# Performance work log

Hardware: AMD Instinct MI355X
Metric: run time of the kernel (lower is better)

## Reference

```python
import jax, jax.numpy as jnp
import numpy as np

N = 131072   # total utterances (nodes)
B = 2048     # conversations (segments)
F = 200      # n_features (hard-coded 200 in source)
STEPS = 3    # processing_steps (reason_steps[0])


def setup_inputs() -> dict:
    key = jax.random.key(0)
    k = jax.random.split(key, 8)
    x = jax.random.normal(k[0], (N, F), dtype=jnp.float32)
    batch = jnp.sort(jax.random.randint(k[1], (N,), 0, B, dtype=jnp.int32))
    cos_coef = jax.random.normal(k[2], (N,), dtype=jnp.float32)
    q_star = jax.random.normal(k[3], (B, 2 * F), dtype=jnp.float32)
    s = 1.0 / np.sqrt(F)
    # PyTorch LSTM params: gate order i, f, g, o; input size 2F, hidden F
    W_ih = jax.random.uniform(k[4], (4 * F, 2 * F), jnp.float32, -s, s)
    W_hh = jax.random.uniform(k[5], (4 * F, F), jnp.float32, -s, s)
    b_ih = jax.random.uniform(k[6], (4 * F,), jnp.float32, -s, s)
    b_hh = jax.random.uniform(k[7], (4 * F,), jnp.float32, -s, s)
    return {"x": x, "batch": batch, "cos_coef": cos_coef, "q_star": q_star,
            "W_ih": W_ih, "W_hh": W_hh, "b_ih": b_ih, "b_hh": b_hh}


def _lstm_cell(inp, h, c, W_ih, W_hh, b_ih, b_hh):
    gates = inp @ W_ih.T + b_ih + h @ W_hh.T + b_hh  # [B, 4F]
    i, f, g, o = jnp.split(gates, 4, axis=-1)
    c = jax.nn.sigmoid(f) * c + jax.nn.sigmoid(i) * jnp.tanh(g)
    h = jax.nn.sigmoid(o) * jnp.tanh(c)
    return h, c


def reference(x, batch, cos_coef, q_star, W_ih, W_hh, b_ih, b_hh):
    # initial LSTM hidden: a_sit[i] = cos_row_i @ x[segment_i]  -> segment_sum
    h = jax.ops.segment_sum(cos_coef[:, None] * x, batch, num_segments=B)  # [B,F]
    c = jnp.zeros((B, F), dtype=x.dtype)
    for _ in range(STEPS):
        h, c = _lstm_cell(q_star, h, c, W_ih, W_hh, b_ih, b_hh)
        q = h                                            # [B,F]
        e = jnp.sum(x * q[batch], axis=-1)               # [N]
        m = jax.ops.segment_max(e, batch, num_segments=B)
        ex = jnp.exp(e - m[batch])
        denom = jax.ops.segment_sum(ex, batch, num_segments=B)
        a = ex / denom[batch]                            # per-segment softmax
        r = jax.ops.segment_sum(a[:, None] * x, batch, num_segments=B)  # [B,F]
        q_star = jnp.concatenate([q, r], axis=-1)        # [B,2F]
    return q_star
```

## Files before the change

### kernel.cpp

```cpp
#include <hip/hip_runtime.h>
#include <hip/hip_bf16.h>

#define N_NODES 131072
#define B_SEG   2048
#define F_DIM   200
#define K_DIM   608
#define NEG_INF (-3.4e38f)
#define NMAX    512

typedef __attribute__((ext_vector_type(8))) short bf16x8;
typedef __attribute__((ext_vector_type(4))) float f32x4;

__device__ __forceinline__ float b2f(unsigned short u) {
  union { unsigned int i; float f; } v; v.i = ((unsigned int)u) << 16; return v.f;
}
__device__ __forceinline__ unsigned short f2bu(float f) {
  __hip_bfloat16 h = __float2bfloat16(f);
  return *reinterpret_cast<unsigned short*>(&h);
}
__device__ __forceinline__ float sigmoidf_(float x) { return 1.f / (1.f + __expf(-x)); }
__device__ __forceinline__ float tanhf_(float x) {
  float e = __expf(2.f * x);
  return 1.f - 2.f / (1.f + e);
}
__device__ __forceinline__ int lower_bound_batch(const int* __restrict__ batch, int target) {
  int lo = 0, hi = N_NODES;
  while (lo < hi) {
    int mid = (lo + hi) >> 1;
    if (batch[mid] < target) lo = mid + 1; else hi = mid;
  }
  return lo;
}

__global__ __launch_bounds__(256) void init_kernel(
    const float* __restrict__ xf, const int* __restrict__ batch,
    const float* __restrict__ cosc, const float* __restrict__ qs0,
    const float* __restrict__ Wih, const float* __restrict__ Whh,
    const float* __restrict__ bih, const float* __restrict__ bhh,
    unsigned short* __restrict__ A, unsigned short* __restrict__ Wc,
    float* __restrict__ bsum, int* __restrict__ seg_off) {
  __shared__ float rpart[5][F_DIM];
  __shared__ float cw[NMAX];
  __shared__ int sb[2];
  int b = blockIdx.x, tid = threadIdx.x;
  if (tid < 2) sb[tid] = lower_bound_batch(batch, b + tid);
  int idx = b * 256 + tid;
  if (idx < 832 * K_DIM) {
    int row = idx / K_DIM, k = idx - row * K_DIM;
    float v = 0.f;
    if (row < 800) {
      if (k < 400)      v = Wih[row * 400 + k];
      else if (k < 600) v = Whh[row * 200 + (k - 400)];
    }
    Wc[idx] = f2bu(v);
  }
  if (idx < 800) bsum[idx] = bih[idx] + bhh[idx];
  __syncthreads();
  int start = sb[0], end = sb[1];
  int n = end - start; if (n > NMAX) n = NMAX;
  if (tid == 0) {
    seg_off[b] = start;
    if (b == 0) seg_off[B_SEG] = N_NODES;
  }
  for (int r = tid; r < n; r += 256) cw[r] = cosc[start + r];
  __syncthreads();
  unsigned short* Arow = A + (size_t)b * K_DIM;
  int rgrp = tid / 50, col4 = tid - rgrp * 50;
  float a0 = 0.f, a1 = 0.f, a2 = 0.f, a3 = 0.f;
  if (rgrp < 5) {
    const float* xp = xf + (size_t)start * F_DIM + 4 * col4;
    int r = rgrp;
    float4 v = {0.f, 0.f, 0.f, 0.f};
    if (r < n) v = *(const float4*)(xp + (size_t)r * F_DIM);
    for (; r < n; r += 5) {
      float4 vc = v;
      int rn = r + 5;
      if (rn < n) v = *(const float4*)(xp + (size_t)rn * F_DIM);
      float cv = cw[r];
      a0 += cv * vc.x; a1 += cv * vc.y; a2 += cv * vc.z; a3 += cv * vc.w;
    }
    rpart[rgrp][4 * col4]     = a0;
    rpart[rgrp][4 * col4 + 1] = a1;
    rpart[rgrp][4 * col4 + 2] = a2;
    rpart[rgrp][4 * col4 + 3] = a3;
  }
  if (tid < 100) {
    float4 v = *(const float4*)(qs0 + (size_t)b * 400 + 4 * tid);
    ushort4 o; o.x = f2bu(v.x); o.y = f2bu(v.y); o.z = f2bu(v.z); o.w = f2bu(v.w);
    *(ushort4*)(Arow + 4 * tid) = o;
  }
  if (tid < 8) Arow[600 + tid] = 0;
  __syncthreads();
  if (tid < F_DIM) {
    float acc = rpart[0][tid] + rpart[1][tid] + rpart[2][tid] + rpart[3][tid]
              + rpart[4][tid];
    Arow[400 + tid] = f2bu(acc);
  }
}

__global__ __launch_bounds__(256) void gemm_gates(
    const unsigned short* __restrict__ A, const unsigned short* __restrict__ W,
    float* __restrict__ gates) {
  int tid = threadIdx.x;
  int bm = blockIdx.x * 32, bn = blockIdx.y * 64;
  int wave = tid >> 6, lane = tid & 63;
  int quad = lane >> 4, col = lane & 15;
  int strip = wave >> 1;
  int tp = (wave & 1) * 2;
  f32x4 acc[2];
  acc[0] = (f32x4){0.f, 0.f, 0.f, 0.f};
  acc[1] = (f32x4){0.f, 0.f, 0.f, 0.f};
  const unsigned short* Ap = A + (size_t)(bm + strip * 16 + col) * K_DIM + quad * 8;
  const unsigned short* Wp = W + (size_t)(bn + col) * K_DIM + quad * 8;
#pragma unroll
  for (int k0 = 0; k0 < K_DIM; k0 += 32) {
    bf16x8 af = *(const bf16x8*)(Ap + k0);
#pragma unroll
    for (int t = 0; t < 2; t++) {
      bf16x8 bfr = *(const bf16x8*)(Wp + (size_t)(tp + t) * 16 * K_DIM + k0);
      acc[t] = __builtin_amdgcn_mfma_f32_16x16x32_bf16(af, bfr, acc[t], 0, 0, 0);
    }
  }
#pragma unroll
  for (int t = 0; t < 2; t++) {
    int gn = bn + (tp + t) * 16 + col;
    if (gn < 800) {
#pragma unroll
      for (int r = 0; r < 4; r++) {
        int gm = bm + strip * 16 + quad * 4 + r;
        gates[(size_t)gm * 800 + gn] = acc[t][r];
      }
    }
  }
}

__global__ __launch_bounds__(256) void attn_fused(
    const float* __restrict__ xf, const int* __restrict__ seg_off,
    const float* __restrict__ gates, const float* __restrict__ bsum,
    float* __restrict__ cvec, unsigned short* __restrict__ A,
    float* __restrict__ out, int step) {
  __shared__ float q_s[F_DIM];
  __shared__ float rpart[8][F_DIM];
  __shared__ float redm[8], redl[8];
  int b = blockIdx.x, tid = threadIdx.x;
  int start = seg_off[b], end = seg_off[b + 1];
  int n = end - start;
  unsigned short* Arow = A + (size_t)b * K_DIM;
  if (tid < F_DIM) {
    int f = tid;
    const float* g = gates + (size_t)b * 800;
    float gi = g[f]       + bsum[f];
    float gf = g[200 + f] + bsum[200 + f];
    float gg = g[400 + f] + bsum[400 + f];
    float go = g[600 + f] + bsum[600 + f];
    float cp = (step > 0) ? cvec[(size_t)b * F_DIM + f] : 0.f;
    float cn = sigmoidf_(gf) * cp + sigmoidf_(gi) * tanhf_(gg);
    float hn = sigmoidf_(go) * tanhf_(cn);
    cvec[(size_t)b * F_DIM + f] = cn;
    q_s[f] = hn;
    if (step < 2) {
      unsigned short hb = f2bu(hn);
      Arow[f] = hb;
      Arow[400 + f] = hb;
    }
  }
  __syncthreads();
  int wave = tid >> 6, lane = tid & 63;
  int half = lane >> 5, hl = lane & 31;
  int hw = wave * 2 + half;
  bool act = (hl < 25);
  float q0=0,q1=0,q2=0,q3=0,q4=0,q5=0,q6=0,q7=0;
  if (act) {
    q0 = q_s[8*hl];   q1 = q_s[8*hl+1]; q2 = q_s[8*hl+2]; q3 = q_s[8*hl+3];
    q4 = q_s[8*hl+4]; q5 = q_s[8*hl+5]; q6 = q_s[8*hl+6]; q7 = q_s[8*hl+7];
  }
  const float* xp = xf + (size_t)start * F_DIM + 8 * hl;
  float m = NEG_INF, l = 0.f;
  float a0=0,a1=0,a2=0,a3=0,a4=0,a5=0,a6=0,a7=0;
  int r = hw;
  float4 va = {0.f,0.f,0.f,0.f}, vb = {0.f,0.f,0.f,0.f};
  if (act && r < n) {
    va = *(const float4*)(xp + (size_t)r * F_DIM);
    vb = *(const float4*)(xp + (size_t)r * F_DIM + 4);
  }
  for (; r < n; r += 8) {
    float4 ca = va, cb = vb;
    int rn = r + 8;
    if (act && rn < n) {
      va = *(const float4*)(xp + (size_t)rn * F_DIM);
      vb = *(const float4*)(xp + (size_t)rn * F_DIM + 4);
    }
    float p = act ? (q0*ca.x + q1*ca.y + q2*ca.z + q3*ca.w
                   + q4*cb.x + q5*cb.y + q6*cb.z + q7*cb.w) : 0.f;
#pragma unroll
    for (int off = 16; off; off >>= 1) p += __shfl_xor(p, off, 32);
    float e = p;
    float mn = fmaxf(m, e);
    float fac = __expf(m - mn);
    float w  = __expf(e - mn);
    l  = l * fac + w;
    a0 = a0*fac + w*ca.x; a1 = a1*fac + w*ca.y; a2 = a2*fac + w*ca.z; a3 = a3*fac + w*ca.w;
    a4 = a4*fac + w*cb.x; a5 = a5*fac + w*cb.y; a6 = a6*fac + w*cb.z; a7 = a7*fac + w*cb.w;
    m = mn;
  }
  if (hl == 0) redm[hw] = m;
  __syncthreads();
  float M = fmaxf(fmaxf(fmaxf(redm[0], redm[1]), fmaxf(redm[2], redm[3])),
                  fmaxf(fmaxf(redm[4], redm[5]), fmaxf(redm[6], redm[7])));
  float facw = (m > NEG_INF) ? __expf(m - M) : 0.f;
  if (hl == 0) redl[hw] = l * facw;
  if (act) {
    float* rp = &rpart[hw][8 * hl];
    rp[0] = a0*facw; rp[1] = a1*facw; rp[2] = a2*facw; rp[3] = a3*facw;
    rp[4] = a4*facw; rp[5] = a5*facw; rp[6] = a6*facw; rp[7] = a7*facw;
  }
  __syncthreads();
  float L = redl[0]+redl[1]+redl[2]+redl[3]+redl[4]+redl[5]+redl[6]+redl[7];
  float inv = (L > 0.f) ? 1.f / L : 0.f;
  if (tid < F_DIM) {
    float rv = (rpart[0][tid]+rpart[1][tid]+rpart[2][tid]+rpart[3][tid]
              + rpart[4][tid]+rpart[5][tid]+rpart[6][tid]+rpart[7][tid]) * inv;
    if (step < 2) {
      Arow[200 + tid] = f2bu(rv);
    } else {
      out[(size_t)b * 400 + tid]       = q_s[tid];
      out[(size_t)b * 400 + 200 + tid] = rv;
    }
  }
}

extern "C" void kernel_launch(void* const* d_in, const int* in_sizes, int n_in,
                              void* d_out, int out_size, void* d_ws, size_t ws_size,
                              hipStream_t stream) {
  const float* x    = (const float*)d_in[0];
  const int*   batch= (const int*)d_in[1];
  const float* cosc = (const float*)d_in[2];
  const float* qs0  = (const float*)d_in[3];
  const float* Wih  = (const float*)d_in[4];
  const float* Whh  = (const float*)d_in[5];
  const float* bih  = (const float*)d_in[6];
  const float* bhh  = (const float*)d_in[7];
  char* ws = (char*)d_ws;
  unsigned short* A    = (unsigned short*)(ws);
  unsigned short* Wc   = (unsigned short*)(ws + 2490368);
  float*          gates= (float*)(ws + 3502080);
  float*          cvec = (float*)(ws + 10055680);
  float*          bsum = (float*)(ws + 11694080);
  int*            soff = (int*)(ws + 11697280);
  float*          outp = (float*)d_out;

  init_kernel<<<B_SEG, 256, 0, stream>>>(x, batch, cosc, qs0, Wih, Whh, bih, bhh,
                                         A, Wc, bsum, soff);
  for (int s = 0; s < 3; s++) {
    gemm_gates<<<dim3(64, 13), 256, 0, stream>>>(A, Wc, gates);
    attn_fused<<<B_SEG, 256, 0, stream>>>(x, soff, gates, bsum, cvec, A, outp, s);
  }
}
```

Baseline: 283.0 us.

## Cache bf16 copy of x in first attention pass and reuse in later steps

The first attention step now writes a bf16 copy of x to workspace while streaming fp32 x, and the later two steps read the bf16 copy. This is meant to cut the memory traffic of the bandwidth-bound attention passes. It adds a 52 MB write and enlarges workspace, and it lowers the precision of x in later steps' logits and weighted sums. The step-0 check becomes a template parameter and the final-step cvec store is skipped.

```diff
diff --git a/kernel.cpp b/kernel.cpp
--- a/kernel.cpp
+++ b/kernel.cpp
@@ -134,8 +134,10 @@
   }
 }
 
+template <int STEP0>
 __global__ __launch_bounds__(256) void attn_fused(
-    const float* __restrict__ xf, const int* __restrict__ seg_off,
+    const float* __restrict__ xf, unsigned short* __restrict__ xb,
+    const int* __restrict__ seg_off,
     const float* __restrict__ gates, const float* __restrict__ bsum,
     float* __restrict__ cvec, unsigned short* __restrict__ A,
     float* __restrict__ out, int step) {
@@ -153,10 +155,10 @@
     float gf = g[200 + f] + bsum[200 + f];
     float gg = g[400 + f] + bsum[400 + f];
     float go = g[600 + f] + bsum[600 + f];
-    float cp = (step > 0) ? cvec[(size_t)b * F_DIM + f] : 0.f;
+    float cp = STEP0 ? 0.f : cvec[(size_t)b * F_DIM + f];
     float cn = sigmoidf_(gf) * cp + sigmoidf_(gi) * tanhf_(gg);
     float hn = sigmoidf_(go) * tanhf_(cn);
-    cvec[(size_t)b * F_DIM + f] = cn;
+    if (step < 2) cvec[(size_t)b * F_DIM + f] = cn;
     q_s[f] = hn;
     if (step < 2) {
       unsigned short hb = f2bu(hn);
@@ -174,34 +176,67 @@
     q0 = q_s[8*hl];   q1 = q_s[8*hl+1]; q2 = q_s[8*hl+2]; q3 = q_s[8*hl+3];
     q4 = q_s[8*hl+4]; q5 = q_s[8*hl+5]; q6 = q_s[8*hl+6]; q7 = q_s[8*hl+7];
   }
-  const float* xp = xf + (size_t)start * F_DIM + 8 * hl;
   float m = NEG_INF, l = 0.f;
   float a0=0,a1=0,a2=0,a3=0,a4=0,a5=0,a6=0,a7=0;
-  int r = hw;
-  float4 va = {0.f,0.f,0.f,0.f}, vb = {0.f,0.f,0.f,0.f};
-  if (act && r < n) {
-    va = *(const float4*)(xp + (size_t)r * F_DIM);
-    vb = *(const float4*)(xp + (size_t)r * F_DIM + 4);
-  }
-  for (; r < n; r += 8) {
-    float4 ca = va, cb = vb;
-    int rn = r + 8;
-    if (act && rn < n) {
-      va = *(const float4*)(xp + (size_t)rn * F_DIM);
-      vb = *(const float4*)(xp + (size_t)rn * F_DIM + 4);
-    }
-    float p = act ? (q0*ca.x + q1*ca.y + q2*ca.z + q3*ca.w
-                   + q4*cb.x + q5*cb.y + q6*cb.z + q7*cb.w) : 0.f;
-#pragma unroll
-    for (int off = 16; off; off >>= 1) p += __shfl_xor(p, off, 32);
-    float e = p;
-    float mn = fmaxf(m, e);
-    float fac = __expf(m - mn);
-    float w  = __expf(e - mn);
-    l  = l * fac + w;
-    a0 = a0*fac + w*ca.x; a1 = a1*fac + w*ca.y; a2 = a2*fac + w*ca.z; a3 = a3*fac + w*ca.w;
-    a4 = a4*fac + w*cb.x; a5 = a5*fac + w*cb.y; a6 = a6*fac + w*cb.z; a7 = a7*fac + w*cb.w;
-    m = mn;
+  if (STEP0) {
+    const float* xp = xf + (size_t)start * F_DIM + 8 * hl;
+    unsigned short* xw = xb + (size_t)start * F_DIM + 8 * hl;
+    int r = hw;
+    float4 va = {0.f,0.f,0.f,0.f}, vb = {0.f,0.f,0.f,0.f};
+    if (act && r < n) {
+      va = *(const float4*)(xp + (size_t)r * F_DIM);
+      vb = *(const float4*)(xp + (size_t)r * F_DIM + 4);
+    }
+    for (; r < n; r += 8) {
+      float4 ca = va, cb = vb;
+      int rn = r + 8;
+      if (act && rn < n) {
+        va = *(const float4*)(xp + (size_t)rn * F_DIM);
+        vb = *(const float4*)(xp + (size_t)rn * F_DIM + 4);
+      }
+      if (act) {
+        ushort4 o0, o1;
+        o0.x = f2bu(ca.x); o0.y = f2bu(ca.y); o0.z = f2bu(ca.z); o0.w = f2bu(ca.w);
+        o1.x = f2bu(cb.x); o1.y = f2bu(cb.y); o1.z = f2bu(cb.z); o1.w = f2bu(cb.w);
+        *(ushort4*)(xw + (size_t)r * F_DIM)     = o0;
+        *(ushort4*)(xw + (size_t)r * F_DIM + 4) = o1;
+      }
+      float p = act ? (q0*ca.x + q1*ca.y + q2*ca.z + q3*ca.w
+                     + q4*cb.x + q5*cb.y + q6*cb.z + q7*cb.w) : 0.f;
+#pragma unroll
+      for (int off = 16; off; off >>= 1) p += __shfl_xor(p, off, 32);
+      float mn = fmaxf(m, p);
+      float fac = __expf(m - mn);
+      float w  = __expf(p - mn);
+      l  = l * fac + w;
+      a0 = a0*fac + w*ca.x; a1 = a1*fac + w*ca.y; a2 = a2*fac + w*ca.z; a3 = a3*fac + w*ca.w;
+      a4 = a4*fac + w*cb.x; a5 = a5*fac + w*cb.y; a6 = a6*fac + w*cb.z; a7 = a7*fac + w*cb.w;
+      m = mn;
+    }
+  } else {
+    const unsigned short* xp = xb + (size_t)start * F_DIM + 8 * hl;
+    int r = hw;
+    uint4 v = {0u, 0u, 0u, 0u};
+    if (act && r < n) v = *(const uint4*)(xp + (size_t)r * F_DIM);
+    for (; r < n; r += 8) {
+      uint4 vc = v;
+      int rn = r + 8;
+      if (act && rn < n) v = *(const uint4*)(xp + (size_t)rn * F_DIM);
+      float x0 = b2f((unsigned short)(vc.x & 0xffff)), x1 = b2f((unsigned short)(vc.x >> 16));
+      float x2 = b2f((unsigned short)(vc.y & 0xffff)), x3 = b2f((unsigned short)(vc.y >> 16));
+      float x4 = b2f((unsigned short)(vc.z & 0xffff)), x5 = b2f((unsigned short)(vc.z >> 16));
+      float x6 = b2f((unsigned short)(vc.w & 0xffff)), x7 = b2f((unsigned short)(vc.w >> 16));
+      float p = act ? (q0*x0 + q1*x1 + q2*x2 + q3*x3 + q4*x4 + q5*x5 + q6*x6 + q7*x7) : 0.f;
+#pragma unroll
+      for (int off = 16; off; off >>= 1) p += __shfl_xor(p, off, 32);
+      float mn = fmaxf(m, p);
+      float fac = __expf(m - mn);
+      float w  = __expf(p - mn);
+      l  = l * fac + w;
+      a0 = a0*fac + w*x0; a1 = a1*fac + w*x1; a2 = a2*fac + w*x2; a3 = a3*fac + w*x3;
+      a4 = a4*fac + w*x4; a5 = a5*fac + w*x5; a6 = a6*fac + w*x6; a7 = a7*fac + w*x7;
+      m = mn;
+    }
   }
   if (hl == 0) redm[hw] = m;
   __syncthreads();
@@ -241,18 +276,22 @@
   const float* bih  = (const float*)d_in[6];
   const float* bhh  = (const float*)d_in[7];
   char* ws = (char*)d_ws;
-  unsigned short* A    = (unsigned short*)(ws);
-  unsigned short* Wc   = (unsigned short*)(ws + 2490368);
-  float*          gates= (float*)(ws + 3502080);
-  float*          cvec = (float*)(ws + 10055680);
-  float*          bsum = (float*)(ws + 11694080);
-  int*            soff = (int*)(ws + 11697280);
+  unsigned short* xb   = (unsigned short*)(ws);
+  unsigned short* A    = (unsigned short*)(ws + 52428800);
+  unsigned short* Wc   = (unsigned short*)(ws + 54919168);
+  float*          gates= (float*)(ws + 55930880);
+  float*          cvec = (float*)(ws + 62484480);
+  float*          bsum = (float*)(ws + 64122880);
+  int*            soff = (int*)(ws + 64126080);
   float*          outp = (float*)d_out;
 
   init_kernel<<<B_SEG, 256, 0, stream>>>(x, batch, cosc, qs0, Wih, Whh, bih, bhh,
                                          A, Wc, bsum, soff);
   for (int s = 0; s < 3; s++) {
     gemm_gates<<<dim3(64, 13), 256, 0, stream>>>(A, Wc, gates);
-    attn_fused<<<B_SEG, 256, 0, stream>>>(x, soff, gates, bsum, cvec, A, outp, s);
-  }
-}
+    if (s == 0)
+      attn_fused<1><<<B_SEG, 256, 0, stream>>>(x, xb, soff, gates, bsum, cvec, A, outp, s);
+    else
+      attn_fused<0><<<B_SEG, 256, 0, stream>>>(x, xb, soff, gates, bsum, cvec, A, outp, s);
+  }
+}
```

After: 275.4 us. 2.7% less time.
